# Kernel optimization log

Measured on AMD Instinct MI355X. Metric: run time of the kernel, lower is better.

## Reference

```python
import jax, jax.numpy as jnp
import numpy as np

B, C, H, W = 32, 64, 96, 96
RED = 8


def setup_inputs() -> dict:
    key = jax.random.key(0)
    k0, k1, k2 = jax.random.split(key, 3)
    x = jax.random.normal(k0, (B, C, H, W), dtype=jnp.float32)
    # 1x1 conv weights (squeezed to linear): conv1 C->C//RED, conv2 C//RED->C
    w1 = jax.random.normal(k1, (C // RED, C), dtype=jnp.float32) * (1.0 / np.sqrt(C))
    b1 = jnp.zeros((C // RED,), dtype=jnp.float32)
    w2 = jax.random.normal(k2, (C, C // RED), dtype=jnp.float32) * (1.0 / np.sqrt(C // RED))
    b2 = jnp.zeros((C,), dtype=jnp.float32)
    return {"x": x, "w1": w1, "b1": b1, "w2": w2, "b2": b2}


def reference(x, w1, b1, w2, b2):
    Bx, Cx, Hx, Wx = x.shape
    M = Hx * Wx
    # --- covariance pooling: x @ I_hat @ x^T == centered outer product / M ---
    xr = x.reshape(Bx, Cx, M)
    xc = xr - xr.mean(axis=-1, keepdims=True)
    cov = jnp.einsum('bcm,bdm->bcd', xc, xc) / M  # (B, C, C)
    # --- Newton-Schulz matrix sqrt, iteration = 5 ---
    I3 = 3.0 * jnp.eye(Cx, dtype=x.dtype)  # broadcast over batch
    normA = jnp.trace(cov, axis1=1, axis2=2)  # (1/3 * cov * 3I).sum == trace
    A = cov / normA[:, None, None]
    ZY = 0.5 * (I3 - A)
    Y = A @ ZY
    Z = ZY
    for _ in range(3):  # range(1, iteration-1) with iteration=5
        ZY = (0.5 * (I3 - Z)) @ Y
        Y = Y @ ZY
        Z = ZY @ Z
    ZY = 0.5 * (Y @ (I3 - Z @ Y))
    cov_sqrt = ZY * jnp.sqrt(normA)[:, None, None]  # (B, C, C)
    # --- channel gating ---
    s = cov_sqrt.mean(axis=1)  # mean over dim=1 -> (B, C)
    h = jax.nn.relu(s @ w1.T + b1)
    gate = jax.nn.sigmoid(h @ w2.T + b2)  # (B, C)
    return x * gate[:, :, None, None]
```

## Files before the change

### kernel.cpp

```cpp
#include <hip/hip_runtime.h>
#include <math.h>


#define BB 32
#define CC 64
#define MM 9216
#define NCHUNKS 16

typedef __attribute__((ext_vector_type(8))) short bf16x8;
typedef __attribute__((ext_vector_type(4))) float f32x4;

__device__ __forceinline__ short f2bf(float f) {
  unsigned u = __builtin_bit_cast(unsigned, f);
  return (short)(unsigned short)((u + 0x8000u) >> 16);
}
__device__ __forceinline__ float bf2f(short h) {
  unsigned u = ((unsigned)(unsigned short)h) << 16;
  return __builtin_bit_cast(float, u);
}
__device__ __forceinline__ void wt_store(float* p, float v) {
  __hip_atomic_store(p, v, __ATOMIC_RELAXED, __HIP_MEMORY_SCOPE_AGENT);
}
__device__ __forceinline__ float ag_load(const float* p) {
  return __hip_atomic_load(p, __ATOMIC_RELAXED, __HIP_MEMORY_SCOPE_AGENT);
}
__device__ __forceinline__ float2 ag_load2(const float* p) {
  unsigned long long u = __hip_atomic_load((const unsigned long long*)p,
                                           __ATOMIC_RELAXED,
                                           __HIP_MEMORY_SCOPE_AGENT);
  return __builtin_bit_cast(float2, u);
}

template <int NSTEP>
__device__ __forceinline__ void gram_body(const float* __restrict__ xb, int mwave,
                                          int quad, int col,
                                          f32x4 acc[4][4], float csum[4]) {
  const float* base[4];
#pragma unroll
  for (int rb = 0; rb < 4; rb++)
    base[rb] = xb + (size_t)(rb * 16 + col) * MM + mwave + quad * 8;

  float4 cur[4][2];
#pragma unroll
  for (int rb = 0; rb < 4; rb++) {
    cur[rb][0] = *(const float4*)(base[rb]);
    cur[rb][1] = *(const float4*)(base[rb] + 4);
  }
#pragma unroll
  for (int s = 0; s < NSTEP; s++) {
    float4 nxt[4][2];
    if (s + 1 < NSTEP) {
#pragma unroll
      for (int rb = 0; rb < 4; rb++) {
        const float* p = base[rb] + (s + 1) * 32;
        nxt[rb][0] = *(const float4*)(p);
        nxt[rb][1] = *(const float4*)(p + 4);
      }
    }
    bf16x8 frag[4];
#pragma unroll
    for (int rb = 0; rb < 4; rb++) {
      float v0 = cur[rb][0].x, v1 = cur[rb][0].y, v2 = cur[rb][0].z, v3 = cur[rb][0].w;
      float v4 = cur[rb][1].x, v5 = cur[rb][1].y, v6 = cur[rb][1].z, v7 = cur[rb][1].w;
      csum[rb] += ((v0 + v1) + (v2 + v3)) + ((v4 + v5) + (v6 + v7));
      bf16x8 f;
      f[0] = f2bf(v0); f[1] = f2bf(v1); f[2] = f2bf(v2); f[3] = f2bf(v3);
      f[4] = f2bf(v4); f[5] = f2bf(v5); f[6] = f2bf(v6); f[7] = f2bf(v7);
      frag[rb] = f;
    }
#pragma unroll
    for (int i = 0; i < 4; i++)
#pragma unroll
      for (int j = 0; j < 4; j++)
        acc[i][j] = __builtin_amdgcn_mfma_f32_16x16x32_bf16(frag[i], frag[j],
                                                            acc[i][j], 0, 0, 0);
    if (s + 1 < NSTEP) {
#pragma unroll
      for (int rb = 0; rb < 4; rb++) {
        cur[rb][0] = nxt[rb][0];
        cur[rb][1] = nxt[rb][1];
      }
    }
  }
}

__device__ __forceinline__ void mm64(short* __restrict__ D, const short* __restrict__ A,
                                     const short* __restrict__ Bm, int tid) {
  int w = tid >> 6, lane = tid & 63, quad = lane >> 4, col = lane & 15;
  f32x4 acc[4];
#pragma unroll
  for (int j = 0; j < 4; j++) acc[j] = (f32x4){0.f, 0.f, 0.f, 0.f};
#pragma unroll
  for (int ks = 0; ks < 2; ks++) {
    int k0 = ks * 32 + quad * 8;
    bf16x8 fa = *(const bf16x8*)(A + (w * 16 + col) * 64 + k0);
#pragma unroll
    for (int j = 0; j < 4; j++) {
      bf16x8 fb = *(const bf16x8*)(Bm + (j * 16 + col) * 64 + k0);
      acc[j] = __builtin_amdgcn_mfma_f32_16x16x32_bf16(fa, fb, acc[j], 0, 0, 0);
    }
  }
#pragma unroll
  for (int j = 0; j < 4; j++)
#pragma unroll
    for (int r = 0; r < 4; r++)
      D[(w * 16 + quad * 4 + r) * 64 + j * 16 + col] = f2bf(acc[j][r]);
}

__device__ __forceinline__ void mmcolsum(const short* __restrict__ A,
                                         const short* __restrict__ Bm,
                                         float* scol, int tid) {
  int w = tid >> 6, lane = tid & 63, quad = lane >> 4, col = lane & 15;
  f32x4 acc[4];
#pragma unroll
  for (int j = 0; j < 4; j++) acc[j] = (f32x4){0.f, 0.f, 0.f, 0.f};
#pragma unroll
  for (int ks = 0; ks < 2; ks++) {
    int k0 = ks * 32 + quad * 8;
    bf16x8 fa = *(const bf16x8*)(A + (w * 16 + col) * 64 + k0);
#pragma unroll
    for (int j = 0; j < 4; j++) {
      bf16x8 fb = *(const bf16x8*)(Bm + (j * 16 + col) * 64 + k0);
      acc[j] = __builtin_amdgcn_mfma_f32_16x16x32_bf16(fa, fb, acc[j], 0, 0, 0);
    }
  }
#pragma unroll
  for (int j = 0; j < 4; j++) {
    float t = (acc[j][0] + acc[j][1]) + (acc[j][2] + acc[j][3]);
    atomicAdd(&scol[j * 16 + col], t);
  }
}

#define GATE_SH_OFF 57920

__device__ __forceinline__ void ns_tail(unsigned char* smem, int b, int tid,
                                        const float* __restrict__ pg,
                                        const float* __restrict__ ps,
                                        const float* __restrict__ w1,
                                        const float* __restrict__ pb1,
                                        const float* __restrict__ w2,
                                        const float* __restrict__ pb2,
                                        float* __restrict__ gatews) {
  short* nb0 = (short*)smem;
  short* nb1 = nb0 + 4096;
  short* nb2 = nb0 + 8192;
  short* nb3 = nb0 + 12288;
  short* nb4 = nb0 + 16384;
  float* gsum = (float*)(smem + 40960);
  float* mu = (float*)(smem + 57344);
  float* scol = (float*)(smem + 57600);
  float* hbuf = (float*)(smem + 57856);
  float* pnorm = (float*)(smem + 57888);
  float* gate_sh = (float*)(smem + GATE_SH_OFF);

  {
    const float* pgb = pg + (size_t)b * NCHUNKS * 4096;
#pragma unroll
    for (int e = 0; e < 8; e++) {
      int i2 = tid + 256 * e;
      float sx = 0.f, sy = 0.f;
#pragma unroll
      for (int c = 0; c < NCHUNKS; c++) {
        float2 v = ag_load2(pgb + c * 4096 + 2 * i2);
        sx += v.x; sy += v.y;
      }
      gsum[2 * i2] = sx;
      gsum[2 * i2 + 1] = sy;
    }
    if (tid < 64) {
      const float* psb = ps + (size_t)b * NCHUNKS * 256;
      float s = 0.f;
#pragma unroll
      for (int c = 0; c < NCHUNKS; c++)
#pragma unroll
        for (int sub = 0; sub < 4; sub++)
          s += ag_load(psb + c * 256 + sub * 64 + tid);
      mu[tid] = s * (1.0f / MM);
    }
  }
  __syncthreads();

  if (tid < 64) {
    float d = gsum[tid * 65] * (1.0f / MM) - mu[tid] * mu[tid];
#pragma unroll
    for (int off = 32; off >= 1; off >>= 1) d += __shfl_down(d, off);
    if (tid == 0) *pnorm = d;
  }
  __syncthreads();
  float normA = *pnorm;
  float rn = 1.0f / normA;
#pragma unroll
  for (int e = 0; e < 16; e++) {
    int idx = tid + 256 * e;
    int r = idx >> 6, c = idx & 63;
    float cv = gsum[idx] * (1.0f / MM) - mu[r] * mu[c];
    float a = cv * rn;
    nb0[idx] = f2bf(a);
    nb1[idx] = f2bf((r == c ? 1.5f : 0.0f) - 0.5f * a);
  }
  __syncthreads();
  mm64(nb2, nb0, nb1, tid);
  __syncthreads();
  short *pY = nb2, *pZ = nb1, *s0 = nb3, *s1 = nb4, *s2 = nb0;
  for (int it = 0; it < 3; ++it) {
#pragma unroll
    for (int e = 0; e < 16; e++) {
      int idx = tid + 256 * e;
      int r = idx >> 6, c = idx & 63;
      float z = bf2f(pZ[idx]);
      s0[idx] = f2bf((r == c ? 1.5f : 0.0f) - 0.5f * z);
    }
    __syncthreads();
    mm64(s1, s0, pY, tid);
    __syncthreads();
    mm64(s2, pY, s1, tid);
    mm64(s0, s1, pZ, tid);
    __syncthreads();
    short* oY = pY; short* oZ = pZ; short* oW = s1;
    pY = s2; pZ = s0; s0 = oY; s1 = oZ; s2 = oW;
  }
  mm64(s0, pZ, pY, tid);
  __syncthreads();
#pragma unroll
  for (int e = 0; e < 16; e++) {
    int idx = tid + 256 * e;
    int r = idx >> 6, c = idx & 63;
    float p = bf2f(s0[idx]);
    s0[idx] = f2bf((r == c ? 3.0f : 0.0f) - p);
  }
  if (tid < 64) scol[tid] = 0.0f;
  __syncthreads();
  mmcolsum(pY, s0, scol, tid);
  __syncthreads();
  if (tid < 8) {
    float sc = 0.5f * sqrtf(normA) * (1.0f / 64.0f);
    float acc2 = pb1[tid];
    for (int c = 0; c < 64; c++) acc2 += scol[c] * sc * w1[tid * 64 + c];
    hbuf[tid] = fmaxf(acc2, 0.0f);
  }
  __syncthreads();
  if (tid < 64) {
    float acc2 = pb2[tid];
#pragma unroll
    for (int j = 0; j < 8; j++) acc2 += hbuf[j] * w2[tid * 8 + j];
    float g = 1.0f / (1.0f + __expf(-acc2));
    gate_sh[tid] = g;
    wt_store(gatews + b * 64 + tid, g);
  }
}

template <int W4>
__device__ __forceinline__ void gate_phase(const float* __restrict__ x,
                                           float* __restrict__ out, int b,
                                           int m0, int tid,
                                           const float* gate_sh) {
  const float4* xp = (const float4*)x;
  float4* op = (float4*)out;
  size_t base = (size_t)b * CC * (MM / 4) + (m0 >> 2);
#pragma unroll
  for (int k = 0; k < (64 * W4) / 256; k++) {
    int i = tid + 256 * k;
    int c = i / W4;
    int off = i - c * W4;
    float g = gate_sh[c];
    size_t idx = base + (size_t)c * (MM / 4) + off;
    float4 v = xp[idx];
    v.x *= g; v.y *= g; v.z *= g; v.w *= g;
    op[idx] = v;
  }
}

__global__ __launch_bounds__(256, 2) void fused_k(
    const float* __restrict__ x, float* __restrict__ pg, float* __restrict__ ps,
    int* __restrict__ ctr, int* __restrict__ flag, const float* __restrict__ w1,
    const float* __restrict__ pb1, const float* __restrict__ w2,
    const float* __restrict__ pb2, float* __restrict__ gatews,
    float* __restrict__ out) {
  __shared__ __align__(16) unsigned char smem[65536];
  float(*red)[4096] = reinterpret_cast<float(*)[4096]>(smem);

  int b = blockIdx.x / NCHUNKS;
  int chunk = blockIdx.x % NCHUNKS;
  int tid = threadIdx.x;
  int w = tid >> 6, lane = tid & 63;
  int quad = lane >> 4, col = lane & 15;
  const float* xb = x + (size_t)b * CC * MM;

  f32x4 acc[4][4];
#pragma unroll
  for (int i = 0; i < 4; i++)
#pragma unroll
    for (int j = 0; j < 4; j++) acc[i][j] = (f32x4){0.f, 0.f, 0.f, 0.f};
  float csum[4] = {0.f, 0.f, 0.f, 0.f};

  int m0;
  if (chunk < 8) {
    m0 = chunk * 640;
    gram_body<5>(xb, m0 + w * 160, quad, col, acc, csum);
  } else {
    m0 = 5120 + (chunk - 8) * 512;
    gram_body<4>(xb, m0 + w * 128, quad, col, acc, csum);
  }

#pragma unroll
  for (int rb = 0; rb < 4; rb++) {
    float c0 = csum[rb];
    c0 += __shfl_xor(c0, 16);
    c0 += __shfl_xor(c0, 32);
    if (lane < 16)
      wt_store(ps + (size_t)blockIdx.x * 256 + w * 64 + rb * 16 + lane, c0);
  }

#pragma unroll
  for (int i = 0; i < 4; i++)
#pragma unroll
    for (int j = 0; j < 4; j++)
#pragma unroll
      for (int r = 0; r < 4; r++)
        red[w][(i * 16 + quad * 4 + r) * 64 + j * 16 + col] = acc[i][j][r];
  __syncthreads();
  float* covb = pg + (size_t)blockIdx.x * 4096;
#pragma unroll
  for (int e = 0; e < 16; e++) {
    int idx = tid + 256 * e;
    float v = (red[0][idx] + red[1][idx]) + (red[2][idx] + red[3][idx]);
    wt_store(covb + idx, v);
  }

  __syncthreads();
  volatile int* pold = (int*)smem;
  if (tid == 0)
    *pold = __hip_atomic_fetch_add(ctr + b, 1, __ATOMIC_RELAXED,
                                   __HIP_MEMORY_SCOPE_AGENT);
  __syncthreads();
  int oldv = *pold;
  __syncthreads();

  float* gate_sh = (float*)(smem + GATE_SH_OFF);
  if (oldv == NCHUNKS - 1) {
    ns_tail(smem, b, tid, pg, ps, w1, pb1, w2, pb2, gatews);
    __syncthreads();
    if (tid == 0)
      __hip_atomic_store(flag + b, 1, __ATOMIC_RELAXED,
                         __HIP_MEMORY_SCOPE_AGENT);
  } else {
    if (tid == 0) {
      while (__hip_atomic_load(flag + b, __ATOMIC_RELAXED,
                               __HIP_MEMORY_SCOPE_AGENT) == 0)
        __builtin_amdgcn_s_sleep(8);
    }
    __syncthreads();
    if (tid < 64) gate_sh[tid] = ag_load(gatews + b * 64 + tid);
    __syncthreads();
  }

  if (chunk < 8)
    gate_phase<160>(x, out, b, m0, tid, gate_sh);
  else
    gate_phase<128>(x, out, b, m0, tid, gate_sh);
}

__global__ __launch_bounds__(256, 2) void gram_k_leg(const float* __restrict__ x,
                                                     float* __restrict__ pg,
                                                     float* __restrict__ ps) {
  int b = blockIdx.x / NCHUNKS;
  int chunk = blockIdx.x % NCHUNKS;
  int tid = threadIdx.x;
  int w = tid >> 6, lane = tid & 63;
  int quad = lane >> 4, col = lane & 15;
  const float* xb = x + (size_t)b * CC * MM;

  f32x4 acc[4][4];
#pragma unroll
  for (int i = 0; i < 4; i++)
#pragma unroll
    for (int j = 0; j < 4; j++) acc[i][j] = (f32x4){0.f, 0.f, 0.f, 0.f};
  float csum[4] = {0.f, 0.f, 0.f, 0.f};
  if (chunk < 8) {
    gram_body<5>(xb, chunk * 640 + w * 160, quad, col, acc, csum);
  } else {
    gram_body<4>(xb, 5120 + (chunk - 8) * 512 + w * 128, quad, col, acc, csum);
  }
#pragma unroll
  for (int rb = 0; rb < 4; rb++) {
    float c0 = csum[rb];
    c0 += __shfl_xor(c0, 16);
    c0 += __shfl_xor(c0, 32);
    if (lane < 16)
      ps[(size_t)blockIdx.x * 256 + w * 64 + rb * 16 + lane] = c0;
  }
  __shared__ float red[4][4096];
#pragma unroll
  for (int i = 0; i < 4; i++)
#pragma unroll
    for (int j = 0; j < 4; j++)
#pragma unroll
      for (int r = 0; r < 4; r++)
        red[w][(i * 16 + quad * 4 + r) * 64 + j * 16 + col] = acc[i][j][r];
  __syncthreads();
  float* covb = pg + (size_t)blockIdx.x * 4096;
#pragma unroll
  for (int e = 0; e < 16; e++) {
    int idx = tid + 256 * e;
    covb[idx] = (red[0][idx] + red[1][idx]) + (red[2][idx] + red[3][idx]);
  }
}

__global__ __launch_bounds__(256) void ns_k_leg(const float* __restrict__ pg,
                                                const float* __restrict__ ps,
                                                const float* __restrict__ w1,
                                                const float* __restrict__ pb1,
                                                const float* __restrict__ w2,
                                                const float* __restrict__ pb2,
                                                float* __restrict__ gatews) {
  __shared__ __align__(16) unsigned char smem[60416];
  ns_tail(smem, blockIdx.x, threadIdx.x, pg, ps, w1, pb1, w2, pb2, gatews);
}

__global__ __launch_bounds__(256) void gate_mul_leg(const float* __restrict__ x,
                                                    const float* __restrict__ gatews,
                                                    float* __restrict__ out) {
  int bc = blockIdx.x;
  float g = gatews[bc];
  const float4* xp = (const float4*)(x + (size_t)bc * MM);
  float4* op = (float4*)(out + (size_t)bc * MM);
  int t = threadIdx.x;
#pragma unroll
  for (int it = 0; it < 9; ++it) {
    float4 v = xp[t + it * 256];
    v.x *= g; v.y *= g; v.z *= g; v.w *= g;
    op[t + it * 256] = v;
  }
}

extern "C" void kernel_launch(void* const* d_in, const int* in_sizes, int n_in,
                              void* d_out, int out_size, void* d_ws, size_t ws_size,
                              hipStream_t stream) {
  const float* x = (const float*)d_in[0];
  const float* w1 = (const float*)d_in[1];
  const float* b1 = (const float*)d_in[2];
  const float* w2 = (const float*)d_in[3];
  const float* b2 = (const float*)d_in[4];
  float* out = (float*)d_out;
  float* ws = (float*)d_ws;

  const size_t NPG = (size_t)BB * NCHUNKS * 4096;
  const size_t NPS = (size_t)BB * NCHUNKS * 256;
  float* pg = ws;
  float* psum = ws + NPG;
  float* gatews = psum + NPS;
  int* ctr = (int*)(gatews + BB * CC);
  int* flag = ctr + BB;
  const size_t needP = (NPG + NPS + BB * CC + 2 * BB) * sizeof(float);

  if (ws_size >= needP) {
    hipMemsetAsync(ctr, 0, 2 * BB * sizeof(int), stream);
    fused_k<<<BB * NCHUNKS, 256, 0, stream>>>(x, pg, psum, ctr, flag, w1, b1,
                                              w2, b2, gatews, out);
  } else {
    gram_k_leg<<<BB * NCHUNKS, 256, 0, stream>>>(x, pg, psum);
    ns_k_leg<<<BB, 256, 0, stream>>>(pg, psum, w1, b1, w2, b2, gatews);
    gate_mul_leg<<<BB * CC, 256, 0, stream>>>(x, gatews, out);
  }
}
```

Measured before the change: 169.3 us.

## Halve LDS reduction buffer to fit three blocks per CU

Shrinks the shared-memory footprint of the fused kernel from 64 KB to about 42 KB. It does this by having waves 2-3 accumulate into the buffers written by waves 0-1, adding an extra barrier, and by repacking the Newton-Schulz scratch layout. The launch bound is raised so three blocks can be resident per CU, which improves latency hiding for the streaming Gram phase. A scheduling barrier is also added in the Gram loop to keep prefetch loads ahead of the conversions, at the risk of register pressure under the tighter occupancy bound.

```diff
diff --git a/kernel.cpp b/kernel.cpp
--- a/kernel.cpp
+++ b/kernel.cpp
@@ -6,6 +6,10 @@
 #define CC 64
 #define MM 9216
 #define NCHUNKS 16
+
+#define SMEM_BYTES 43008
+#define GATE_SH_OFF 41536
+#define POLD_OFF 41856
 
 typedef __attribute__((ext_vector_type(8))) short bf16x8;
 typedef __attribute__((ext_vector_type(4))) float f32x4;
@@ -57,6 +61,7 @@
         nxt[rb][1] = *(const float4*)(p + 4);
       }
     }
+    __builtin_amdgcn_sched_barrier(0);
     bf16x8 frag[4];
 #pragma unroll
     for (int rb = 0; rb < 4; rb++) {
@@ -130,8 +135,6 @@
     atomicAdd(&scol[j * 16 + col], t);
   }
 }
-
-#define GATE_SH_OFF 57920
 
 __device__ __forceinline__ void ns_tail(unsigned char* smem, int b, int tid,
                                         const float* __restrict__ pg,
@@ -146,11 +149,11 @@
   short* nb2 = nb0 + 8192;
   short* nb3 = nb0 + 12288;
   short* nb4 = nb0 + 16384;
-  float* gsum = (float*)(smem + 40960);
-  float* mu = (float*)(smem + 57344);
-  float* scol = (float*)(smem + 57600);
-  float* hbuf = (float*)(smem + 57856);
-  float* pnorm = (float*)(smem + 57888);
+  float* gsum = (float*)(smem + 16384);
+  float* mu = (float*)(smem + 40960);
+  float* scol = (float*)(smem + 41216);
+  float* hbuf = (float*)(smem + 41472);
+  float* pnorm = (float*)(smem + 41504);
   float* gate_sh = (float*)(smem + GATE_SH_OFF);
 
   {
@@ -270,13 +273,13 @@
   }
 }
 
-__global__ __launch_bounds__(256, 2) void fused_k(
+__global__ __launch_bounds__(256, 3) void fused_k(
     const float* __restrict__ x, float* __restrict__ pg, float* __restrict__ ps,
     int* __restrict__ ctr, int* __restrict__ flag, const float* __restrict__ w1,
     const float* __restrict__ pb1, const float* __restrict__ w2,
     const float* __restrict__ pb2, float* __restrict__ gatews,
     float* __restrict__ out) {
-  __shared__ __align__(16) unsigned char smem[65536];
+  __shared__ __align__(16) unsigned char smem[SMEM_BYTES];
   float(*red)[4096] = reinterpret_cast<float(*)[4096]>(smem);
 
   int b = blockIdx.x / NCHUNKS;
@@ -311,24 +314,35 @@
       wt_store(ps + (size_t)blockIdx.x * 256 + w * 64 + rb * 16 + lane, c0);
   }
 
-#pragma unroll
-  for (int i = 0; i < 4; i++)
-#pragma unroll
-    for (int j = 0; j < 4; j++)
-#pragma unroll
-      for (int r = 0; r < 4; r++)
-        red[w][(i * 16 + quad * 4 + r) * 64 + j * 16 + col] = acc[i][j][r];
+  if (w < 2) {
+#pragma unroll
+    for (int i = 0; i < 4; i++)
+#pragma unroll
+      for (int j = 0; j < 4; j++)
+#pragma unroll
+        for (int r = 0; r < 4; r++)
+          red[w][(i * 16 + quad * 4 + r) * 64 + j * 16 + col] = acc[i][j][r];
+  }
+  __syncthreads();
+  if (w >= 2) {
+#pragma unroll
+    for (int i = 0; i < 4; i++)
+#pragma unroll
+      for (int j = 0; j < 4; j++)
+#pragma unroll
+        for (int r = 0; r < 4; r++)
+          red[w - 2][(i * 16 + quad * 4 + r) * 64 + j * 16 + col] += acc[i][j][r];
+  }
   __syncthreads();
   float* covb = pg + (size_t)blockIdx.x * 4096;
 #pragma unroll
   for (int e = 0; e < 16; e++) {
     int idx = tid + 256 * e;
-    float v = (red[0][idx] + red[1][idx]) + (red[2][idx] + red[3][idx]);
-    wt_store(covb + idx, v);
-  }
-
-  __syncthreads();
-  volatile int* pold = (int*)smem;
+    wt_store(covb + idx, red[0][idx] + red[1][idx]);
+  }
+
+  __syncthreads();
+  volatile int* pold = (int*)(smem + POLD_OFF);
   if (tid == 0)
     *pold = __hip_atomic_fetch_add(ctr + b, 1, __ATOMIC_RELAXED,
                                    __HIP_MEMORY_SCOPE_AGENT);
@@ -389,20 +403,32 @@
     if (lane < 16)
       ps[(size_t)blockIdx.x * 256 + w * 64 + rb * 16 + lane] = c0;
   }
-  __shared__ float red[4][4096];
-#pragma unroll
-  for (int i = 0; i < 4; i++)
-#pragma unroll
-    for (int j = 0; j < 4; j++)
-#pragma unroll
-      for (int r = 0; r < 4; r++)
-        red[w][(i * 16 + quad * 4 + r) * 64 + j * 16 + col] = acc[i][j][r];
+  __shared__ float red[2][4096];
+  if (w < 2) {
+#pragma unroll
+    for (int i = 0; i < 4; i++)
+#pragma unroll
+      for (int j = 0; j < 4; j++)
+#pragma unroll
+        for (int r = 0; r < 4; r++)
+          red[w][(i * 16 + quad * 4 + r) * 64 + j * 16 + col] = acc[i][j][r];
+  }
+  __syncthreads();
+  if (w >= 2) {
+#pragma unroll
+    for (int i = 0; i < 4; i++)
+#pragma unroll
+      for (int j = 0; j < 4; j++)
+#pragma unroll
+        for (int r = 0; r < 4; r++)
+          red[w - 2][(i * 16 + quad * 4 + r) * 64 + j * 16 + col] += acc[i][j][r];
+  }
   __syncthreads();
   float* covb = pg + (size_t)blockIdx.x * 4096;
 #pragma unroll
   for (int e = 0; e < 16; e++) {
     int idx = tid + 256 * e;
-    covb[idx] = (red[0][idx] + red[1][idx]) + (red[2][idx] + red[3][idx]);
+    covb[idx] = red[0][idx] + red[1][idx];
   }
 }
 
@@ -413,7 +439,7 @@
                                                 const float* __restrict__ w2,
                                                 const float* __restrict__ pb2,
                                                 float* __restrict__ gatews) {
-  __shared__ __align__(16) unsigned char smem[60416];
+  __shared__ __align__(16) unsigned char smem[SMEM_BYTES];
   ns_tail(smem, blockIdx.x, threadIdx.x, pg, ps, w1, pb1, w2, pb2, gatews);
 }
 
```

Result: no change. 168.4 us (-0.5%).
